# Optimization experiments

Hardware: AMD Instinct MI355X
Metric: run time of the kernel (lower is better)

The kernel has to match this reference:

```python
import math
import jax, jax.numpy as jnp
import numpy as np


def _proj(x, w, b):
    # 1x1x1 Conv3d == pointwise channel matmul: (B,C,T,H,W) x (O,C) -> (B,O,T,H,W)
    return jnp.einsum('bcthw,oc->bothw', x, w) + b[None, :, None, None, None]


def setup_inputs() -> dict:
    key = jax.random.key(0)
    ks = jax.random.split(key, 16)
    B, C, T, H, W = 2, 64, 16, 14, 14
    CI = C // 2
    s_in = 1.0 / math.sqrt(C)
    s_out = 1.0 / math.sqrt(CI)
    inp = {'x': jax.random.normal(ks[0], (B, C, T, H, W), jnp.float32)}
    # QKV projections for spatial (s) and temporal (t) branches: (CI, C) weights
    pnames = ['qs', 'ks', 'vs', 'qt', 'kt', 'vt']
    for i, n in enumerate(pnames):
        inp['W' + n] = jax.random.normal(ks[1 + i], (CI, C), jnp.float32) * s_in
        inp['b' + n] = jax.random.normal(ks[7 + i], (CI,), jnp.float32) * 0.01
    # output projection W: (C, CI)
    inp['Ww'] = jax.random.normal(ks[13], (C, CI), jnp.float32) * s_out
    inp['bw'] = jax.random.normal(ks[14], (C,), jnp.float32) * 0.01
    return inp


def reference(x, Wqs, bqs, Wks, bks, Wvs, bvs, Wqt, bqt, Wkt, bkt, Wvt, bvt, Ww, bw):
    B, C, T, H, W = x.shape
    CI = Wqs.shape[0]
    N = CI * H * W  # flat dim after original's raw .view (mixes channel & spatial/time)
    scale = 1.0 / math.sqrt(T)

    # ---- spatial branch: .view(B, T, -1) raw reshape of (B,CI,T,H,W) ----
    qs = _proj(x, Wqs, bqs).reshape(B, T, N).transpose(0, 2, 1)   # (B,N,T)
    ks_ = _proj(x, Wks, bks).reshape(B, T, N)                     # (B,T,N)
    vs = _proj(x, Wvs, bvs).reshape(B, T, N).transpose(0, 2, 1)   # (B,N,T)
    attn_s = jax.nn.softmax(jnp.einsum('bnt,btm->bnm', qs, ks_) * scale, axis=-1)  # (B,N,N)
    ys = jnp.einsum('bnm,bmt->bnt', attn_s, vs)                   # (B,N,T)
    ys = ys.transpose(0, 2, 1).reshape(B, CI, T, H, W)

    # ---- temporal branch: .view(B, CI*H*W, -1) raw reshape ----
    qt = _proj(x, Wqt, bqt).reshape(B, N, T).transpose(0, 2, 1)   # (B,T,N)
    kt = _proj(x, Wkt, bkt).reshape(B, N, T)                      # (B,N,T)
    vt = _proj(x, Wvt, bvt).reshape(B, N, T).transpose(0, 2, 1)   # (B,T,N)
    attn_t = jax.nn.softmax(jnp.einsum('btn,bns->bts', qt, kt) * scale, axis=-1)  # (B,T,T)
    yt = jnp.einsum('bts,bsn->btn', attn_t, vt)                   # (B,T,N)
    yt = yt.transpose(0, 2, 1).reshape(B, CI, T, H, W)

    y = ys + yt
    return _proj(y, Ww, bw) + x
```

## Files before the change

### kernel.cpp

```cpp
#include <hip/hip_runtime.h>
#include <math.h>

#define S3   3136
#define PB   100352
#define XB   200704
#define NN   6272
#define MW   7
#define MPW  896
#define TGC  49

typedef __attribute__((ext_vector_type(8))) short bf16x8;
typedef __attribute__((ext_vector_type(16))) float f32x16;
typedef __attribute__((ext_vector_type(4))) uint u32x4;

__device__ inline ushort f2bf(float f) {
    uint u = __float_as_uint(f);
    return (ushort)((u + 0x7FFFu + ((u >> 16) & 1u)) >> 16);
}

__device__ inline uint cvtpk(float lo, float hi) {
    uint r;
    asm("v_cvt_pk_bf16_f32 %0, %1, %2" : "=v"(r) : "v"(lo), "v"(hi));
    return r;
}

__device__ inline void swap32(uint &a, uint &b) {
    asm("v_permlane32_swap_b32 %0, %1" : "+v"(a), "+v"(b));
}

__global__ __launch_bounds__(256) void proj_kernel(
    const float* __restrict__ x,
    const float* __restrict__ W0, const float* __restrict__ b0,
    const float* __restrict__ W1, const float* __restrict__ b1,
    const float* __restrict__ W2, const float* __restrict__ b2,
    const float* __restrict__ W3, const float* __restrict__ b3,
    const float* __restrict__ W4, const float* __restrict__ b4,
    const float* __restrict__ W5, const float* __restrict__ b5,
    ushort* __restrict__ Qb, ushort* __restrict__ Kb, ushort* __restrict__ Vb,
    float* __restrict__ Qt, float* __restrict__ Kt, float* __restrict__ Vt)
{
    const float* Wp; const float* bp;
    switch (blockIdx.y) {
        case 0:  Wp = W0; bp = b0; break;
        case 1:  Wp = W1; bp = b1; break;
        case 2:  Wp = W2; bp = b2; break;
        case 3:  Wp = W3; bp = b3; break;
        case 4:  Wp = W4; bp = b4; break;
        default: Wp = W5; bp = b5; break;
    }
    int z = blockIdx.z;

    int gid = blockIdx.x * 256 + threadIdx.x;
    if (gid >= 2 * S3) return;
    int b = (gid >= S3) ? 1 : 0;
    int s = gid - b * S3;

    float xr[64];
    #pragma unroll
    for (int c = 0; c < 64; ++c) xr[c] = x[(size_t)b * XB + (size_t)c * S3 + s];

    float a[4];
    #pragma unroll
    for (int oo = 0; oo < 4; ++oo) {
        int o = z * 4 + oo;
        float acc = bp[o];
        #pragma unroll
        for (int c = 0; c < 64; ++c) acc = fmaf(Wp[o * 64 + c], xr[c], acc);
        a[oo] = acc;
    }

    if (blockIdx.y < 2) {
        const float sc = (blockIdx.y == 0) ? 0.36067376022224085f : 1.0f;
        ushort* ob = (blockIdx.y == 0) ? Qb : Kb;
        #pragma unroll
        for (int h = 0; h < 2; ++h) {
            int n = h * S3 + s;
            uint u0 = f2bf(a[0 + h] * sc) | ((uint)f2bf(a[2 + h] * sc) << 16);
            *(uint*)(ob + ((size_t)(b * NN + n) * 16 + z * 2)) = u0;
        }
    } else if (blockIdx.y == 2) {
        #pragma unroll
        for (int oo = 0; oo < 4; ++oo) {
            int o = z * 4 + oo;
            Vb[(size_t)(b * 16 + (o >> 1)) * NN + (o & 1) * S3 + s] = f2bf(a[oo]);
        }
    } else {
        float* op = (blockIdx.y == 3) ? Qt : (blockIdx.y == 4) ? Kt : Vt;
        #pragma unroll
        for (int oo = 0; oo < 4; ++oo)
            op[(size_t)b * PB + (size_t)(z * 4 + oo) * S3 + s] = a[oo];
    }
}

__global__ __launch_bounds__(256) void attn_kernel(
    const ushort* __restrict__ Qb, const ushort* __restrict__ Kb,
    const ushort* __restrict__ Vb, const float* __restrict__ Qt,
    const float* __restrict__ Kt,
    float* __restrict__ Pacc, float* __restrict__ Pl, float* __restrict__ Gp)
{
    __shared__ float qs[128 * 16], ks[128 * 16];

    int b = blockIdx.y;

    if (blockIdx.x >= 343) {
        int c = blockIdx.x - 343;
        size_t base = (size_t)b * PB + (size_t)c * 2048;
        for (int i = threadIdx.x; i < 512; i += 256) {
            ((float4*)qs)[i] = ((const float4*)(Qt + base))[i];
            ((float4*)ks)[i] = ((const float4*)(Kt + base))[i];
        }
        __syncthreads();
        int t = threadIdx.x >> 4, s = threadIdx.x & 15;
        float acc = 0.0f;
        #pragma unroll 8
        for (int n = 0; n < 128; ++n)
            acc = fmaf(qs[n * 16 + t], ks[n * 16 + s], acc);
        Gp[(size_t)(b * TGC + c) * 256 + threadIdx.x] = acc;
        return;
    }

    int wave = __builtin_amdgcn_readfirstlane((int)(threadIdx.x >> 6));
    int lane = threadIdx.x & 63;
    int col  = lane & 31;
    int h    = lane >> 5;
    int gw   = blockIdx.x * 4 + wave;
    int ntile = gw / 7;
    int w     = gw - ntile * 7;
    int nbase = ntile * 32;
    int m0    = w * MPW;

    bf16x8 qf = *(const bf16x8*)(Qb + ((size_t)(b * NN + nbase + col) * 16 + h * 8));

    const bf16x8 vzero = {0, 0, 0, 0, 0, 0, 0, 0};
    const bf16x8 vones = {16256, 16256, 16256, 16256, 16256, 16256, 16256, 16256};
    f32x16 yacc;
    #pragma unroll
    for (int r = 0; r < 16; ++r) yacc[r] = 0.0f;
    f32x16 zero16 = yacc;

    #pragma unroll 2
    for (int it = 0; it < MPW / 32; ++it) {
        int mb = m0 + it * 32;
        bf16x8 kf = *(const bf16x8*)(Kb + ((size_t)(b * NN + mb + col) * 16 + h * 8));
        bf16x8 vf0 = vzero, vf1 = vzero;
        if (col < 16) {
            const ushort* vp = Vb + ((size_t)(b * 16 + col) * NN + mb + h * 8);
            vf0 = *(const bf16x8*)(vp);
            vf1 = *(const bf16x8*)(vp + 16);
        } else if (col == 16) { vf0 = vones; vf1 = vones; }

        f32x16 st = __builtin_amdgcn_mfma_f32_32x32x16_bf16(kf, qf, zero16, 0, 0, 0);
        float pv[16];
        #pragma unroll
        for (int r = 0; r < 16; ++r) pv[r] = __builtin_amdgcn_exp2f(st[r]);

        uint X0 = cvtpk(pv[0],  pv[1]),  X1 = cvtpk(pv[2],  pv[3]);
        uint Y0 = cvtpk(pv[4],  pv[5]),  Y1 = cvtpk(pv[6],  pv[7]);
        uint X2 = cvtpk(pv[8],  pv[9]),  X3 = cvtpk(pv[10], pv[11]);
        uint Y2 = cvtpk(pv[12], pv[13]), Y3 = cvtpk(pv[14], pv[15]);
        swap32(X0, Y0); swap32(X1, Y1);
        swap32(X2, Y2); swap32(X3, Y3);
        u32x4 pb0 = {X0, X1, Y0, Y1};
        u32x4 pb1 = {X2, X3, Y2, Y3};

        yacc = __builtin_amdgcn_mfma_f32_32x32x16_bf16(
                   vf0, __builtin_bit_cast(bf16x8, pb0), yacc, 0, 0, 0);
        yacc = __builtin_amdgcn_mfma_f32_32x32x16_bf16(
                   vf1, __builtin_bit_cast(bf16x8, pb1), yacc, 0, 0, 0);
    }

    #pragma unroll
    for (int r = 0; r < 8; ++r) {
        int t = (r & 3) + 8 * (r >> 2) + 4 * h;
        Pacc[((size_t)(b * 16 + t) * MW + w) * NN + nbase + col] = yacc[r];
    }
    if (h == 0)
        Pl[((size_t)b * MW + w) * NN + nbase + col] = yacc[8];
}

__global__ __launch_bounds__(256) void merge_final(
    const float* __restrict__ Pacc, const float* __restrict__ Pl,
    const float* __restrict__ Gp, const float* __restrict__ Vt,
    const float* __restrict__ x, const float* __restrict__ Ww,
    const float* __restrict__ bw, float* __restrict__ out)
{
    __shared__ float Lsh[256];
    __shared__ float Ash[16][17];
    __shared__ float Wsh[64 * 36];
    __shared__ float Ysh[8 * 36];

    int b  = blockIdx.y;
    int sc = blockIdx.x;

    {
        float a = 0.0f;
        for (int c = 0; c < TGC; ++c)
            a += Gp[(size_t)(b * TGC + c) * 256 + threadIdx.x];
        Lsh[threadIdx.x] = a * 0.25f;
        for (int i = threadIdx.x; i < 2048; i += 256)
            Wsh[(i >> 5) * 36 + (i & 31)] = Ww[i];
    }
    __syncthreads();
    if (threadIdx.x < 16) {
        int t = threadIdx.x;
        const float* Lr = &Lsh[t * 16];
        float mx = -1e30f;
        #pragma unroll
        for (int s = 0; s < 16; ++s) mx = fmaxf(mx, Lr[s]);
        float e[16]; float sm = 0.0f;
        #pragma unroll
        for (int s = 0; s < 16; ++s) { e[s] = __expf(Lr[s] - mx); sm += e[s]; }
        float inv = 1.0f / sm;
        #pragma unroll
        for (int s = 0; s < 16; ++s) Ash[s][t] = e[s] * inv;
    }
    __syncthreads();

    {
        int idx = threadIdx.x;
        int ss = idx & 7;
        int ci = idx >> 3;
        int s  = sc * 8 + ss;
        int t  = ci >> 1;
        int nn = (ci & 1) * S3 + s;

        float a = 0.0f, l = 0.0f;
        #pragma unroll
        for (int w = 0; w < MW; ++w) {
            a += Pacc[((size_t)(b * 16 + t) * MW + w) * NN + nn];
            l += Pl[((size_t)b * MW + w) * NN + nn];
        }
        float ys = a / l;

        int t2 = nn & 15;
        const float4* vp = (const float4*)(Vt + (size_t)b * PB + (size_t)t * NN + (nn & ~15));
        float4 v0 = vp[0], v1 = vp[1], v2 = vp[2], v3 = vp[3];
        float yt = Ash[0][t2] * v0.x;
        yt = fmaf(Ash[1][t2],  v0.y, yt); yt = fmaf(Ash[2][t2],  v0.z, yt);
        yt = fmaf(Ash[3][t2],  v0.w, yt); yt = fmaf(Ash[4][t2],  v1.x, yt);
        yt = fmaf(Ash[5][t2],  v1.y, yt); yt = fmaf(Ash[6][t2],  v1.z, yt);
        yt = fmaf(Ash[7][t2],  v1.w, yt); yt = fmaf(Ash[8][t2],  v2.x, yt);
        yt = fmaf(Ash[9][t2],  v2.y, yt); yt = fmaf(Ash[10][t2], v2.z, yt);
        yt = fmaf(Ash[11][t2], v2.w, yt); yt = fmaf(Ash[12][t2], v3.x, yt);
        yt = fmaf(Ash[13][t2], v3.y, yt); yt = fmaf(Ash[14][t2], v3.z, yt);
        yt = fmaf(Ash[15][t2], v3.w, yt);

        Ysh[ss * 36 + ci] = ys + yt;
    }
    __syncthreads();

    int ss = threadIdx.x & 7;
    int cg = threadIdx.x >> 3;
    int s  = sc * 8 + ss;

    float acc[2];
    #pragma unroll
    for (int k = 0; k < 2; ++k) acc[k] = bw[cg * 2 + k];

    #pragma unroll
    for (int cb = 0; cb < 32; cb += 4) {
        float4 y4 = *(const float4*)&Ysh[ss * 36 + cb];
        #pragma unroll
        for (int k = 0; k < 2; ++k) {
            float4 w4 = *(const float4*)&Wsh[(cg * 2 + k) * 36 + cb];
            acc[k] = fmaf(w4.x, y4.x, acc[k]);
            acc[k] = fmaf(w4.y, y4.y, acc[k]);
            acc[k] = fmaf(w4.z, y4.z, acc[k]);
            acc[k] = fmaf(w4.w, y4.w, acc[k]);
        }
    }

    #pragma unroll
    for (int k = 0; k < 2; ++k) {
        int c = cg * 2 + k;
        size_t o = (size_t)b * XB + (size_t)c * S3 + s;
        out[o] = x[o] + acc[k];
    }
}

extern "C" void kernel_launch(void* const* d_in, const int* in_sizes, int n_in,
                              void* d_out, int out_size, void* d_ws, size_t ws_size,
                              hipStream_t stream)
{
    const float* x   = (const float*)d_in[0];
    const float* Wqs = (const float*)d_in[1];  const float* bqs = (const float*)d_in[2];
    const float* Wks = (const float*)d_in[3];  const float* bks = (const float*)d_in[4];
    const float* Wvs = (const float*)d_in[5];  const float* bvs = (const float*)d_in[6];
    const float* Wqt = (const float*)d_in[7];  const float* bqt = (const float*)d_in[8];
    const float* Wkt = (const float*)d_in[9];  const float* bkt = (const float*)d_in[10];
    const float* Wvt = (const float*)d_in[11]; const float* bvt = (const float*)d_in[12];
    const float* Ww  = (const float*)d_in[13]; const float* bw  = (const float*)d_in[14];

    float* ws = (float*)d_ws;
    ushort* Qb = (ushort*)(ws);
    ushort* Kb = (ushort*)(ws + 100352);
    ushort* Vb = (ushort*)(ws + 200704);
    float* Qt  = ws + 301056;
    float* Kt  = ws + 501760;
    float* Vt  = ws + 702464;
    float* Gp  = ws + 903168;
    float* Pacc = ws + 928256;
    float* Pl   = ws + 2333184;

    proj_kernel<<<dim3(25, 6, 8), 256, 0, stream>>>(
        x, Wqs, bqs, Wks, bks, Wvs, bvs, Wqt, bqt, Wkt, bkt, Wvt, bvt,
        Qb, Kb, Vb, Qt, Kt, Vt);

    attn_kernel<<<dim3(343 + TGC, 2), 256, 0, stream>>>(
        Qb, Kb, Vb, Qt, Kt, Pacc, Pl, Gp);

    merge_final<<<dim3(392, 2), 256, 0, stream>>>(
        Pacc, Pl, Gp, Vt, x, Ww, bw, (float*)d_out);
}
```

Measured before the change: 125.2 us.

## Fuse spatial attention with merge and output projection, reducing split-KV partials in LDS

The split-KV partial accumulators (Pacc/Pl) are no longer written to global memory and reduced in a separate merge kernel. Each 512-thread block now handles 32 query rows: its 8 waves stride over all key tiles, reduce their partials through shared memory, and then apply the temporal-branch mix, output projection and residual in the same block. The Gram partials move into their own small kernel launched before this one. This removes a large global round-trip and one kernel boundary, but it adds an extra launch and leaves each fused block with a long serial loop over the key tiles.

Result: no change. 125.0 us (median of 2 runs) (-0.2%).

```diff
diff --git a/kernel.cpp b/kernel.cpp
--- a/kernel.cpp
+++ b/kernel.cpp
@@ -5,8 +5,6 @@
 #define PB   100352
 #define XB   200704
 #define NN   6272
-#define MW   7
-#define MPW  896
 #define TGC  49
 
 typedef __attribute__((ext_vector_type(8))) short bf16x8;
@@ -92,44 +90,75 @@
     }
 }
 
-__global__ __launch_bounds__(256) void attn_kernel(
+__global__ __launch_bounds__(256) void gram_kernel(
+    const float* __restrict__ Qt, const float* __restrict__ Kt,
+    float* __restrict__ Gp)
+{
+    __shared__ float qs[128 * 16], ks[128 * 16];
+    int b = blockIdx.y;
+    int c = blockIdx.x;
+    size_t base = (size_t)b * PB + (size_t)c * 2048;
+    for (int i = threadIdx.x; i < 512; i += 256) {
+        ((float4*)qs)[i] = ((const float4*)(Qt + base))[i];
+        ((float4*)ks)[i] = ((const float4*)(Kt + base))[i];
+    }
+    __syncthreads();
+    int t = threadIdx.x >> 4, s = threadIdx.x & 15;
+    float acc = 0.0f;
+    #pragma unroll 8
+    for (int n = 0; n < 128; ++n)
+        acc = fmaf(qs[n * 16 + t], ks[n * 16 + s], acc);
+    Gp[(size_t)(b * TGC + c) * 256 + threadIdx.x] = acc;
+}
+
+__global__ __launch_bounds__(512) void attn_merge_kernel(
     const ushort* __restrict__ Qb, const ushort* __restrict__ Kb,
-    const ushort* __restrict__ Vb, const float* __restrict__ Qt,
-    const float* __restrict__ Kt,
-    float* __restrict__ Pacc, float* __restrict__ Pl, float* __restrict__ Gp)
-{
-    __shared__ float qs[128 * 16], ks[128 * 16];
-
-    int b = blockIdx.y;
-
-    if (blockIdx.x >= 343) {
-        int c = blockIdx.x - 343;
-        size_t base = (size_t)b * PB + (size_t)c * 2048;
-        for (int i = threadIdx.x; i < 512; i += 256) {
-            ((float4*)qs)[i] = ((const float4*)(Qt + base))[i];
-            ((float4*)ks)[i] = ((const float4*)(Kt + base))[i];
-        }
-        __syncthreads();
-        int t = threadIdx.x >> 4, s = threadIdx.x & 15;
-        float acc = 0.0f;
-        #pragma unroll 8
-        for (int n = 0; n < 128; ++n)
-            acc = fmaf(qs[n * 16 + t], ks[n * 16 + s], acc);
-        Gp[(size_t)(b * TGC + c) * 256 + threadIdx.x] = acc;
-        return;
-    }
-
-    int wave = __builtin_amdgcn_readfirstlane((int)(threadIdx.x >> 6));
-    int lane = threadIdx.x & 63;
+    const ushort* __restrict__ Vb, const float* __restrict__ Gp,
+    const float* __restrict__ Vt, const float* __restrict__ x,
+    const float* __restrict__ Ww, const float* __restrict__ bw,
+    float* __restrict__ out)
+{
+    __shared__ float Yred[8][17][32];
+    __shared__ float Gpart[2][256];
+    __shared__ float Lsh[256];
+    __shared__ float Ash[16][17];
+    __shared__ float Ysh[32][17];
+
+    int b   = blockIdx.y;
+    int s0  = blockIdx.x * 16;
+    int tid = threadIdx.x;
+
+    {
+        int j = tid & 255, g = tid >> 8;
+        float a = 0.0f;
+        for (int c = g; c < TGC; c += 2)
+            a += Gp[(size_t)(b * TGC + c) * 256 + j];
+        Gpart[g][j] = a;
+    }
+    __syncthreads();
+    if (tid < 256) Lsh[tid] = (Gpart[0][tid] + Gpart[1][tid]) * 0.25f;
+    __syncthreads();
+    if (tid < 16) {
+        int t = tid;
+        const float* Lr = &Lsh[t * 16];
+        float mx = -1e30f;
+        #pragma unroll
+        for (int s = 0; s < 16; ++s) mx = fmaxf(mx, Lr[s]);
+        float e[16]; float sm = 0.0f;
+        #pragma unroll
+        for (int s = 0; s < 16; ++s) { e[s] = __expf(Lr[s] - mx); sm += e[s]; }
+        float inv = 1.0f / sm;
+        #pragma unroll
+        for (int s = 0; s < 16; ++s) Ash[s][t] = e[s] * inv;
+    }
+
+    int wave = __builtin_amdgcn_readfirstlane(tid >> 6);
+    int lane = tid & 63;
     int col  = lane & 31;
     int h    = lane >> 5;
-    int gw   = blockIdx.x * 4 + wave;
-    int ntile = gw / 7;
-    int w     = gw - ntile * 7;
-    int nbase = ntile * 32;
-    int m0    = w * MPW;
-
-    bf16x8 qf = *(const bf16x8*)(Qb + ((size_t)(b * NN + nbase + col) * 16 + h * 8));
+    int nq   = (col >> 4) * S3 + s0 + (col & 15);
+
+    bf16x8 qf = *(const bf16x8*)(Qb + ((size_t)(b * NN + nq) * 16 + h * 8));
 
     const bf16x8 vzero = {0, 0, 0, 0, 0, 0, 0, 0};
     const bf16x8 vones = {16256, 16256, 16256, 16256, 16256, 16256, 16256, 16256};
@@ -138,9 +167,8 @@
     for (int r = 0; r < 16; ++r) yacc[r] = 0.0f;
     f32x16 zero16 = yacc;
 
-    #pragma unroll 2
-    for (int it = 0; it < MPW / 32; ++it) {
-        int mb = m0 + it * 32;
+    for (int i = wave; i < 196; i += 8) {
+        int mb = i * 32;
         bf16x8 kf = *(const bf16x8*)(Kb + ((size_t)(b * NN + mb + col) * 16 + h * 8));
         bf16x8 vf0 = vzero, vf1 = vzero;
         if (col < 16) {
@@ -172,68 +200,26 @@
     #pragma unroll
     for (int r = 0; r < 8; ++r) {
         int t = (r & 3) + 8 * (r >> 2) + 4 * h;
-        Pacc[((size_t)(b * 16 + t) * MW + w) * NN + nbase + col] = yacc[r];
-    }
-    if (h == 0)
-        Pl[((size_t)b * MW + w) * NN + nbase + col] = yacc[8];
-}
-
-__global__ __launch_bounds__(256) void merge_final(
-    const float* __restrict__ Pacc, const float* __restrict__ Pl,
-    const float* __restrict__ Gp, const float* __restrict__ Vt,
-    const float* __restrict__ x, const float* __restrict__ Ww,
-    const float* __restrict__ bw, float* __restrict__ out)
-{
-    __shared__ float Lsh[256];
-    __shared__ float Ash[16][17];
-    __shared__ float Wsh[64 * 36];
-    __shared__ float Ysh[8 * 36];
-
-    int b  = blockIdx.y;
-    int sc = blockIdx.x;
+        Yred[wave][t][col] = yacc[r];
+    }
+    if (h == 0) Yred[wave][16][col] = yacc[8];
+    __syncthreads();
 
     {
-        float a = 0.0f;
-        for (int c = 0; c < TGC; ++c)
-            a += Gp[(size_t)(b * TGC + c) * 256 + threadIdx.x];
-        Lsh[threadIdx.x] = a * 0.25f;
-        for (int i = threadIdx.x; i < 2048; i += 256)
-            Wsh[(i >> 5) * 36 + (i & 31)] = Ww[i];
-    }
-    __syncthreads();
-    if (threadIdx.x < 16) {
-        int t = threadIdx.x;
-        const float* Lr = &Lsh[t * 16];
-        float mx = -1e30f;
-        #pragma unroll
-        for (int s = 0; s < 16; ++s) mx = fmaxf(mx, Lr[s]);
-        float e[16]; float sm = 0.0f;
-        #pragma unroll
-        for (int s = 0; s < 16; ++s) { e[s] = __expf(Lr[s] - mx); sm += e[s]; }
-        float inv = 1.0f / sm;
-        #pragma unroll
-        for (int s = 0; s < 16; ++s) Ash[s][t] = e[s] * inv;
-    }
-    __syncthreads();
-
-    {
-        int idx = threadIdx.x;
-        int ss = idx & 7;
-        int ci = idx >> 3;
-        int s  = sc * 8 + ss;
-        int t  = ci >> 1;
-        int nn = (ci & 1) * S3 + s;
-
-        float a = 0.0f, l = 0.0f;
-        #pragma unroll
-        for (int w = 0; w < MW; ++w) {
-            a += Pacc[((size_t)(b * 16 + t) * MW + w) * NN + nn];
-            l += Pl[((size_t)b * MW + w) * NN + nn];
-        }
-        float ys = a / l;
-
-        int t2 = nn & 15;
-        const float4* vp = (const float4*)(Vt + (size_t)b * PB + (size_t)t * NN + (nn & ~15));
+        int t    = tid >> 5;
+        int c2   = tid & 31;
+        float ysum = 0.0f, lsum = 0.0f;
+        #pragma unroll
+        for (int w = 0; w < 8; ++w) {
+            ysum += Yred[w][t][c2];
+            lsum += Yred[w][16][c2];
+        }
+        float ys = ysum / lsum;
+
+        int t2   = c2 & 15;
+        int half = c2 >> 4;
+        const float4* vp = (const float4*)(Vt + (size_t)b * PB + (size_t)t * NN
+                                           + (size_t)half * S3 + s0);
         float4 v0 = vp[0], v1 = vp[1], v2 = vp[2], v3 = vp[3];
         float yt = Ash[0][t2] * v0.x;
         yt = fmaf(Ash[1][t2],  v0.y, yt); yt = fmaf(Ash[2][t2],  v0.z, yt);
@@ -245,36 +231,29 @@
         yt = fmaf(Ash[13][t2], v3.y, yt); yt = fmaf(Ash[14][t2], v3.z, yt);
         yt = fmaf(Ash[15][t2], v3.w, yt);
 
-        Ysh[ss * 36 + ci] = ys + yt;
-    }
-    __syncthreads();
-
-    int ss = threadIdx.x & 7;
-    int cg = threadIdx.x >> 3;
-    int s  = sc * 8 + ss;
-
-    float acc[2];
-    #pragma unroll
-    for (int k = 0; k < 2; ++k) acc[k] = bw[cg * 2 + k];
-
-    #pragma unroll
-    for (int cb = 0; cb < 32; cb += 4) {
-        float4 y4 = *(const float4*)&Ysh[ss * 36 + cb];
-        #pragma unroll
-        for (int k = 0; k < 2; ++k) {
-            float4 w4 = *(const float4*)&Wsh[(cg * 2 + k) * 36 + cb];
-            acc[k] = fmaf(w4.x, y4.x, acc[k]);
-            acc[k] = fmaf(w4.y, y4.y, acc[k]);
-            acc[k] = fmaf(w4.z, y4.z, acc[k]);
-            acc[k] = fmaf(w4.w, y4.w, acc[k]);
-        }
-    }
-
-    #pragma unroll
-    for (int k = 0; k < 2; ++k) {
-        int c = cg * 2 + k;
-        size_t o = (size_t)b * XB + (size_t)c * S3 + s;
-        out[o] = x[o] + acc[k];
+        Ysh[2 * t + half][t2] = ys + yt;
+    }
+    __syncthreads();
+
+    {
+        int s  = tid & 15;
+        int cg = tid >> 4;
+        #pragma unroll
+        for (int kk = 0; kk < 2; ++kk) {
+            int c = cg + kk * 32;
+            float acc = bw[c];
+            const float4* wr = (const float4*)(Ww + c * 32);
+            #pragma unroll
+            for (int cb = 0; cb < 8; ++cb) {
+                float4 w4 = wr[cb];
+                acc = fmaf(w4.x, Ysh[cb * 4 + 0][s], acc);
+                acc = fmaf(w4.y, Ysh[cb * 4 + 1][s], acc);
+                acc = fmaf(w4.z, Ysh[cb * 4 + 2][s], acc);
+                acc = fmaf(w4.w, Ysh[cb * 4 + 3][s], acc);
+            }
+            size_t o = (size_t)b * XB + (size_t)c * S3 + s0 + s;
+            out[o] = x[o] + acc;
+        }
     }
 }
 
@@ -299,16 +278,13 @@
     float* Kt  = ws + 501760;
     float* Vt  = ws + 702464;
     float* Gp  = ws + 903168;
-    float* Pacc = ws + 928256;
-    float* Pl   = ws + 2333184;
 
     proj_kernel<<<dim3(25, 6, 8), 256, 0, stream>>>(
         x, Wqs, bqs, Wks, bks, Wvs, bvs, Wqt, bqt, Wkt, bkt, Wvt, bvt,
         Qb, Kb, Vb, Qt, Kt, Vt);
 
-    attn_kernel<<<dim3(343 + TGC, 2), 256, 0, stream>>>(
-        Qb, Kb, Vb, Qt, Kt, Pacc, Pl, Gp);
-
-    merge_final<<<dim3(392, 2), 256, 0, stream>>>(
-        Pacc, Pl, Gp, Vt, x, Ww, bw, (float*)d_out);
-}
+    gram_kernel<<<dim3(TGC, 2), 256, 0, stream>>>(Qt, Kt, Gp);
+
+    attn_merge_kernel<<<dim3(196, 2), 512, 0, stream>>>(
+        Qb, Kb, Vb, Gp, Vt, x, Ww, bw, (float*)d_out);
+}
```
